# Optimization experiments

Hardware: AMD Instinct MI355X
Metric: run time of the kernel (lower is better)

## Reference

```python
import jax, jax.numpy as jnp
import numpy as np

NUM_BINS = 16
D_MODEL = 128
TAIL_BOUND = 20.0
MIN_BIN_WIDTH = 1e-3
MIN_BIN_HEIGHT = 1e-3
MIN_DERIVATIVE = 1e-3
EPS = 1e-6


def setup_inputs() -> dict:
    key = jax.random.key(0)
    ks = jax.random.split(key, 10)
    B, S = 32, 8192
    sc = 0.05  # small init scale so spline logits stay moderate
    return {
        "inputs": jax.random.normal(ks[0], (B, S), dtype=jnp.float32),
        "conditioning": jax.random.normal(ks[1], (B, S, D_MODEL), dtype=jnp.float32),
        "Ww": jax.random.normal(ks[2], (NUM_BINS, D_MODEL), dtype=jnp.float32) * sc,
        "bw": jax.random.normal(ks[3], (NUM_BINS,), dtype=jnp.float32) * sc,
        "Wh": jax.random.normal(ks[4], (NUM_BINS, D_MODEL), dtype=jnp.float32) * sc,
        "bh": jax.random.normal(ks[5], (NUM_BINS,), dtype=jnp.float32) * sc,
        "Wd": jax.random.normal(ks[6], (NUM_BINS - 1, D_MODEL), dtype=jnp.float32) * sc,
        "bd": jax.random.normal(ks[7], (NUM_BINS - 1,), dtype=jnp.float32) * sc,
        "Wl": jax.random.normal(ks[8], (NUM_BINS, D_MODEL), dtype=jnp.float32) * sc,
        "bl": jax.random.normal(ks[9], (NUM_BINS,), dtype=jnp.float32) * sc,
    }


def _rational_linear_spline(x, uw, uh, ud, ul, left, right, bottom, top):
    nb = uw.shape[-1]
    # bin widths / cumulative widths
    w = MIN_BIN_WIDTH + (1.0 - MIN_BIN_WIDTH * nb) * jax.nn.softmax(uw, axis=-1)
    cw = jnp.concatenate([jnp.zeros_like(w[..., :1]), jnp.cumsum(w, axis=-1)], axis=-1)
    cw = (right - left) * cw + left
    cw = cw.at[..., 0].set(left).at[..., -1].set(right)
    w = cw[..., 1:] - cw[..., :-1]
    # derivatives (ud already padded to nb+1 by caller)
    d = MIN_DERIVATIVE + jax.nn.softplus(ud)
    # bin heights / cumulative heights
    h = MIN_BIN_HEIGHT + (1.0 - MIN_BIN_HEIGHT * nb) * jax.nn.softmax(uh, axis=-1)
    ch = jnp.concatenate([jnp.zeros_like(h[..., :1]), jnp.cumsum(h, axis=-1)], axis=-1)
    ch = (top - bottom) * ch + bottom
    ch = ch.at[..., 0].set(bottom).at[..., -1].set(top)
    h = ch[..., 1:] - ch[..., :-1]
    # searchsorted via sum of comparisons (as in source)
    locs = cw.at[..., -1].add(EPS)
    idx = jnp.sum((x[..., None] >= locs).astype(jnp.int32), axis=-1) - 1
    idx = jnp.clip(idx, 0, nb - 1)
    g = lambda t: jnp.take_along_axis(t, idx[..., None], axis=-1)[..., 0]
    in_cw = g(cw)
    in_bw = g(w)
    in_ch = g(ch)
    in_delta = g(h / w)
    dk = g(d)
    dk1 = g(d[..., 1:])
    in_h = g(h)
    lambdas = 0.95 * jax.nn.sigmoid(ul) + 0.025
    lam = g(lambdas)
    wa = 1.0
    wb = jnp.sqrt(dk / dk1) * wa
    wc = (lam * wa * dk + (1.0 - lam) * wb * dk1) / in_delta
    ya = in_ch
    yb = in_h + in_ch
    yc = ((1.0 - lam) * wa * ya + lam * wb * yb) / ((1.0 - lam) * wa + lam * wb)
    theta = (x - in_cw) / in_bw
    m = theta <= lam
    num = jnp.where(m, wa * ya * (lam - theta) + wc * yc * theta,
                    wc * yc * (1.0 - theta) + wb * yb * (theta - lam))
    den = jnp.where(m, wa * (lam - theta) + wc * theta,
                    wc * (1.0 - theta) + wb * (theta - lam))
    out = num / den
    deriv_num = jnp.where(m, wa * wc * lam * (yc - ya), wb * wc * (1.0 - lam) * (yb - yc)) / in_bw
    logabsdet = jnp.log(deriv_num) - 2.0 * jnp.log(jnp.abs(den))
    return out, logabsdet


def reference(inputs, conditioning, Ww, bw, Wh, bh, Wd, bd, Wl, bl):
    # parameter nets (module.forward): note the module normalizes here AND the
    # spline normalizes again -- replicate faithfully.
    uw = jax.nn.softmax(jnp.einsum('bsd,kd->bsk', conditioning, Ww) + bw, axis=-1)
    uh = jax.nn.softmax(jnp.einsum('bsd,kd->bsk', conditioning, Wh) + bh, axis=-1)
    ud = jax.nn.softplus(jnp.einsum('bsd,kd->bsk', conditioning, Wd) + bd)
    ul = jax.nn.sigmoid(jnp.einsum('bsd,kd->bsk', conditioning, Wl) + bl)
    # linear tails: pad derivatives with constant so boundary derivative == 1
    const = float(np.log(np.exp(1.0 - MIN_DERIVATIVE) - 1.0))
    edge = jnp.full(ud.shape[:-1] + (1,), const, dtype=ud.dtype)
    udp = jnp.concatenate([edge, ud, edge], axis=-1)  # [B,S,nb+1]
    tb = TAIL_BOUND
    inside = (inputs >= -tb) & (inputs <= tb)
    xc = jnp.clip(inputs, -tb, tb)
    s_out, s_lad = _rational_linear_spline(xc, uw, uh, udp, ul, -tb, tb, -tb, tb)
    outputs = jnp.where(inside, s_out, inputs)
    logabsdet = jnp.where(inside, s_lad, 0.0)
    return outputs, logabsdet
```

## Files before the change

kernel.cpp:

```cpp
#include <hip/hip_runtime.h>
#include <math.h>

#define NB 16
#define DM 128
#define BM 256
#define ZSTRIDE 68

typedef _Float16 half8  __attribute__((ext_vector_type(8)));
typedef _Float16 half4v __attribute__((ext_vector_type(4)));
typedef _Float16 half2v __attribute__((ext_vector_type(2)));
typedef __fp16   fp16x2 __attribute__((ext_vector_type(2)));
typedef float    f32x4  __attribute__((ext_vector_type(4)));

__device__ __forceinline__ float frcp_(float x) { return __builtin_amdgcn_rcpf(x); }
__device__ __forceinline__ float softplus_fast(float x) {
    return fmaxf(x, 0.0f) + __logf(1.0f + __expf(-fabsf(x)));
}
__device__ __forceinline__ float sigmoid_fast(float x) {
    return frcp_(1.0f + __expf(-x));
}
__device__ __forceinline__ void softmax16_m(float* z) {
    float m = z[0];
#pragma unroll
    for (int k = 1; k < NB; k++) m = fmaxf(m, z[k]);
    float s = 0.0f;
#pragma unroll
    for (int k = 0; k < NB; k++) { z[k] = __expf(z[k] - m); s += z[k]; }
    float r = frcp_(s);
#pragma unroll
    for (int k = 0; k < NB; k++) z[k] *= r;
}
__device__ __forceinline__ void softmax16_nm(float* z) {
    float s = 0.0f;
#pragma unroll
    for (int k = 0; k < NB; k++) { z[k] = __expf(z[k]); s += z[k]; }
    float r = frcp_(s);
#pragma unroll
    for (int k = 0; k < NB; k++) z[k] *= r;
}

__device__ __forceinline__ half2v pk_(float lo, float hi) {
    fp16x2 p = __builtin_amdgcn_cvt_pkrtz(lo, hi);
    return __builtin_bit_cast(half2v, p);
}
__device__ __forceinline__ half8 cvt8(float4 a0, float4 a1) {
    half2v p0 = pk_(a0.x, a0.y);
    half2v p1 = pk_(a0.z, a0.w);
    half2v p2 = pk_(a1.x, a1.y);
    half2v p3 = pk_(a1.z, a1.w);
    half8 f;
    f[0] = p0[0]; f[1] = p0[1]; f[2] = p1[0]; f[3] = p1[1];
    f[4] = p2[0]; f[5] = p2[1]; f[6] = p3[0]; f[7] = p3[1];
    return f;
}

#define ISSUE(P, cr, koff)                                  \
    P##0 = *(const float4*)((cr) + (koff));                 \
    P##1 = *(const float4*)((cr) + (koff) + 4);             \
    P##2 = *(const float4*)((cr) + (koff) + 32);            \
    P##3 = *(const float4*)((cr) + (koff) + 36);

#define CVT2(P, lo, hi)                                     \
    lo = cvt8(P##0, P##1);                                  \
    hi = cvt8(P##2, P##3);

#define MFMA_S(af, s)                                                           \
    acc0 = __builtin_amdgcn_mfma_f32_16x16x32_f16(af, B0##s, acc0, 0, 0, 0);    \
    acc1 = __builtin_amdgcn_mfma_f32_16x16x32_f16(af, B1##s, acc1, 0, 0, 0);    \
    acc2 = __builtin_amdgcn_mfma_f32_16x16x32_f16(af, B2##s, acc2, 0, 0, 0);    \
    acc3 = __builtin_amdgcn_mfma_f32_16x16x32_f16(af, B3##s, acc3, 0, 0, 0);

#define STOREZ(c) {                                                             \
    _Float16* zpw = zbase + (size_t)((c) * 16) * ZSTRIDE;                       \
    _Pragma("unroll")                                                           \
    for (int r = 0; r < 4; r++) {                                               \
        half2v p0 = pk_(acc0[r], acc1[r]);                                      \
        half2v p1 = pk_(acc2[r], acc3[r]);                                      \
        half4v w; w[0] = p0[0]; w[1] = p0[1]; w[2] = p1[0]; w[3] = p1[1];       \
        *(half4v*)(zpw + (size_t)r * ZSTRIDE) = w;                              \
    } }

#define RESET_ACC  acc0 = zf4; acc1 = zf4; acc2 = zf4; acc3 = zf4;

#define STAGE_B(Wt, isWd, Q0, Q1, Q2, Q3) {                                     \
    const bool val = (!(isWd)) || (l15 < 15);                                   \
    const float* srcl = (Wt) + (size_t)(val ? l15 : 0) * DM + lg * 8;           \
    float4 q0 = *(const float4*)(srcl + 0),  q1 = *(const float4*)(srcl + 4);   \
    float4 q2 = *(const float4*)(srcl + 32), q3 = *(const float4*)(srcl + 36);  \
    float4 q4 = *(const float4*)(srcl + 64), q5 = *(const float4*)(srcl + 68);  \
    float4 q6 = *(const float4*)(srcl + 96), q7 = *(const float4*)(srcl + 100); \
    Q0 = val ? cvt8(q0, q1) : hz;                                               \
    Q1 = val ? cvt8(q2, q3) : hz;                                               \
    Q2 = val ? cvt8(q4, q5) : hz;                                               \
    Q3 = val ? cvt8(q6, q7) : hz; }

__global__ __launch_bounds__(256, 3) void spline_mfma(
    const float* __restrict__ xin, const float* __restrict__ cond,
    const float* __restrict__ Ww, const float* __restrict__ bw,
    const float* __restrict__ Wh, const float* __restrict__ bh,
    const float* __restrict__ Wd, const float* __restrict__ bd,
    const float* __restrict__ Wl, const float* __restrict__ bl,
    float* __restrict__ out, float* __restrict__ lad, int N)
{
    __shared__ __align__(16) _Float16 Z[BM * ZSTRIDE];

    const int tid  = threadIdx.x;
    const int wave = tid >> 6;
    const int lane = tid & 63;
    const int l15  = lane & 15;
    const int lg   = lane >> 4;
    const size_t blockRow = (size_t)blockIdx.x * BM;

    const size_t gi = blockRow + tid;
    float x = xin[gi < (size_t)N ? gi : 0];

    size_t gr0 = blockRow + (size_t)(wave * 64 + l15);
    size_t gr1 = gr0 + 16, gr2 = gr0 + 32, gr3 = gr0 + 48;
    if (gr0 >= (size_t)N) gr0 = (size_t)N - 1;
    if (gr1 >= (size_t)N) gr1 = (size_t)N - 1;
    if (gr2 >= (size_t)N) gr2 = (size_t)N - 1;
    if (gr3 >= (size_t)N) gr3 = (size_t)N - 1;
    const float* cr0 = cond + gr0 * DM + lg * 8;
    const float* cr1 = cond + gr1 * DM + lg * 8;
    const float* cr2 = cond + gr2 * DM + lg * 8;
    const float* cr3 = cond + gr3 * DM + lg * 8;

    float4 X0, X1, X2, X3, Y0, Y1, Y2, Y3;
    ISSUE(X, cr0, 0)
    ISSUE(Y, cr0, 64)

    half8 hz;
    hz[0]=hz[1]=hz[2]=hz[3]=hz[4]=hz[5]=hz[6]=hz[7] = (_Float16)0.0f;
    half8 B00, B01, B02, B03, B10, B11, B12, B13,
          B20, B21, B22, B23, B30, B31, B32, B33;
    STAGE_B(Ww, false, B00, B01, B02, B03)
    STAGE_B(Wh, false, B10, B11, B12, B13)
    STAGE_B(Wl, false, B20, B21, B22, B23)
    STAGE_B(Wd, true,  B30, B31, B32, B33)

    const f32x4 zf4 = {0.f, 0.f, 0.f, 0.f};
    f32x4 acc0 = zf4, acc1 = zf4, acc2 = zf4, acc3 = zf4;
    half8 af0, af1;
    _Float16* zbase = &Z[(size_t)(wave * 64 + lg * 4) * ZSTRIDE + l15 * 4];

    CVT2(X, af0, af1)
    ISSUE(X, cr1, 0)
    MFMA_S(af0, 0) MFMA_S(af1, 1)
    CVT2(Y, af0, af1)
    ISSUE(Y, cr1, 64)
    MFMA_S(af0, 2) MFMA_S(af1, 3)
    STOREZ(0) RESET_ACC

    CVT2(X, af0, af1)
    ISSUE(X, cr2, 0)
    MFMA_S(af0, 0) MFMA_S(af1, 1)
    CVT2(Y, af0, af1)
    ISSUE(Y, cr2, 64)
    MFMA_S(af0, 2) MFMA_S(af1, 3)
    STOREZ(1) RESET_ACC

    CVT2(X, af0, af1)
    ISSUE(X, cr3, 0)
    MFMA_S(af0, 0) MFMA_S(af1, 1)
    CVT2(Y, af0, af1)
    ISSUE(Y, cr3, 64)
    MFMA_S(af0, 2) MFMA_S(af1, 3)
    STOREZ(2) RESET_ACC

    CVT2(X, af0, af1)
    MFMA_S(af0, 0) MFMA_S(af1, 1)
    CVT2(Y, af0, af1)
    MFMA_S(af0, 2) MFMA_S(af1, 3)
    STOREZ(3)

    __builtin_amdgcn_sched_barrier(0);
    asm volatile("s_waitcnt lgkmcnt(0)" ::: "memory");
    __builtin_amdgcn_sched_barrier(0);

    if (gi >= (size_t)N) return;

    float zw[NB], zh[NB], zl[NB], zd[NB - 1];
    const half4v* zr4 = (const half4v*)&Z[(size_t)tid * ZSTRIDE];
#pragma unroll
    for (int j = 0; j < NB; j++) {
        half4v v = zr4[j];
        zw[j] = (float)v[0] + bw[j];
        zh[j] = (float)v[1] + bh[j];
        zl[j] = (float)v[2] + bl[j];
        if (j < NB - 1) zd[j] = (float)v[3] + bd[j];
    }

    float xc = fminf(fmaxf(x, -20.0f), 20.0f);

    softmax16_m(zw);
    softmax16_nm(zw);
    const float scale = (1.0f - 1e-3f * NB);
    float cw[NB + 1];
    cw[0] = -20.0f;
    float cum = 0.0f;
#pragma unroll
    for (int k = 0; k < NB; k++) {
        cum += 1e-3f + scale * zw[k];
        cw[k + 1] = 40.0f * cum - 20.0f;
    }
    cw[NB] = 20.0f;

    softmax16_m(zh);
    softmax16_nm(zh);
    float ch[NB + 1];
    ch[0] = -20.0f;
    cum = 0.0f;
#pragma unroll
    for (int k = 0; k < NB; k++) {
        cum += 1e-3f + scale * zh[k];
        ch[k + 1] = 40.0f * cum - 20.0f;
    }
    ch[NB] = 20.0f;

    float in_cw = cw[0], cw_hi = cw[1], in_ch = ch[0], ch_hi = ch[1];
    float zl_sel = zl[0], zd_lo = zd[0], zd_hi = zd[0];
#pragma unroll
    for (int k = 1; k < NB; k++) {
        bool take = (xc >= cw[k]);
        in_cw  = take ? cw[k]     : in_cw;
        cw_hi  = take ? cw[k + 1] : cw_hi;
        in_ch  = take ? ch[k]     : in_ch;
        ch_hi  = take ? ch[k + 1] : ch_hi;
        zl_sel = take ? zl[k]     : zl_sel;
        zd_lo  = take ? zd[k - 1] : zd_lo;
        zd_hi  = take ? zd[(k < NB - 1) ? k : NB - 2] : zd_hi;
    }
    bool firstbin = (xc <  cw[1]);
    bool lastbin  = (xc >= cw[NB - 1]);

    float in_bw = cw_hi - in_cw;
    float in_h  = ch_hi - in_ch;

    float dk  = firstbin ? 1.0f : (1e-3f + softplus_fast(softplus_fast(zd_lo)));
    float dk1 = lastbin  ? 1.0f : (1e-3f + softplus_fast(softplus_fast(zd_hi)));

    float ul  = sigmoid_fast(zl_sel);
    float lam = 0.95f * sigmoid_fast(ul) + 0.025f;

    float rbw = frcp_(in_bw);
    float in_delta = in_h * rbw;
    float wb = sqrtf(dk * frcp_(dk1));
    float wc = (lam * dk + (1.0f - lam) * wb * dk1) * frcp_(in_delta);
    float ya = in_ch;
    float yb = in_h + in_ch;
    float yc = ((1.0f - lam) * ya + lam * wb * yb) * frcp_((1.0f - lam) + lam * wb);
    float theta = (xc - in_cw) * rbw;
    bool mlt = (theta <= lam);

    float num = mlt ? (ya * (lam - theta) + wc * yc * theta)
                    : (wc * yc * (1.0f - theta) + wb * yb * (theta - lam));
    float den = mlt ? ((lam - theta) + wc * theta)
                    : (wc * (1.0f - theta) + wb * (theta - lam));
    float sout = num * frcp_(den);
    float dnum = (mlt ? (wc * lam * (yc - ya))
                      : (wb * wc * (1.0f - lam) * (yb - yc))) * rbw;
    float slad = __logf(dnum) - 2.0f * __logf(fabsf(den));

    bool inside = (x >= -20.0f) && (x <= 20.0f);
    out[gi] = inside ? sout : x;
    lad[gi] = inside ? slad : 0.0f;
}

extern "C" void kernel_launch(void* const* d_in, const int* in_sizes, int n_in,
                              void* d_out, int out_size, void* d_ws, size_t ws_size,
                              hipStream_t stream) {
    const float* xin  = (const float*)d_in[0];
    const float* cond = (const float*)d_in[1];
    const float* Ww   = (const float*)d_in[2];
    const float* bwp  = (const float*)d_in[3];
    const float* Wh   = (const float*)d_in[4];
    const float* bhp  = (const float*)d_in[5];
    const float* Wd   = (const float*)d_in[6];
    const float* bdp  = (const float*)d_in[7];
    const float* Wl   = (const float*)d_in[8];
    const float* blp  = (const float*)d_in[9];
    int N = in_sizes[0];
    float* out = (float*)d_out;
    float* lad = out + N;
    int grid = (N + BM - 1) / BM;
    hipLaunchKernelGGL(spline_mfma, dim3(grid), dim3(256), 0, stream,
                       xin, cond, Ww, bwp, Wh, bhp, Wd, bdp, Wl, blp, out, lad, N);
}
```

Baseline: 41.63 us.

## Issue all conditioning loads up front and relax launch bounds to two blocks

Measured after the change: 39.08 us. 1.07x faster.

```diff
diff --git a/kernel.cpp b/kernel.cpp
--- a/kernel.cpp
+++ b/kernel.cpp
@@ -54,15 +54,21 @@
     return f;
 }
 
-#define ISSUE(P, cr, koff)                                  \
-    P##0 = *(const float4*)((cr) + (koff));                 \
-    P##1 = *(const float4*)((cr) + (koff) + 4);             \
-    P##2 = *(const float4*)((cr) + (koff) + 32);            \
-    P##3 = *(const float4*)((cr) + (koff) + 36);
-
-#define CVT2(P, lo, hi)                                     \
-    lo = cvt8(P##0, P##1);                                  \
-    hi = cvt8(P##2, P##3);
+#define LOADC(c)                                        \
+    A##c##_0 = *(const float4*)(cr##c + 0);             \
+    A##c##_1 = *(const float4*)(cr##c + 4);             \
+    A##c##_2 = *(const float4*)(cr##c + 32);            \
+    A##c##_3 = *(const float4*)(cr##c + 36);            \
+    A##c##_4 = *(const float4*)(cr##c + 64);            \
+    A##c##_5 = *(const float4*)(cr##c + 68);            \
+    A##c##_6 = *(const float4*)(cr##c + 96);            \
+    A##c##_7 = *(const float4*)(cr##c + 100);
+
+#define CVTC(c)                                         \
+    af0 = cvt8(A##c##_0, A##c##_1);                     \
+    af1 = cvt8(A##c##_2, A##c##_3);                     \
+    af2 = cvt8(A##c##_4, A##c##_5);                     \
+    af3 = cvt8(A##c##_6, A##c##_7);
 
 #define MFMA_S(af, s)                                                           \
     acc0 = __builtin_amdgcn_mfma_f32_16x16x32_f16(af, B0##s, acc0, 0, 0, 0);    \
@@ -94,7 +100,7 @@
     Q2 = val ? cvt8(q4, q5) : hz;                                               \
     Q3 = val ? cvt8(q6, q7) : hz; }
 
-__global__ __launch_bounds__(256, 3) void spline_mfma(
+__global__ __launch_bounds__(256, 2) void spline_mfma(
     const float* __restrict__ xin, const float* __restrict__ cond,
     const float* __restrict__ Ww, const float* __restrict__ bw,
     const float* __restrict__ Wh, const float* __restrict__ bh,
@@ -110,9 +116,16 @@
     const int l15  = lane & 15;
     const int lg   = lane >> 4;
     const size_t blockRow = (size_t)blockIdx.x * BM;
-
     const size_t gi = blockRow + tid;
-    float x = xin[gi < (size_t)N ? gi : 0];
+
+    half8 hz;
+    hz[0]=hz[1]=hz[2]=hz[3]=hz[4]=hz[5]=hz[6]=hz[7] = (_Float16)0.0f;
+    half8 B00, B01, B02, B03, B10, B11, B12, B13,
+          B20, B21, B22, B23, B30, B31, B32, B33;
+    STAGE_B(Ww, false, B00, B01, B02, B03)
+    STAGE_B(Wh, false, B10, B11, B12, B13)
+    STAGE_B(Wl, false, B20, B21, B22, B23)
+    STAGE_B(Wd, true,  B30, B31, B32, B33)
 
     size_t gr0 = blockRow + (size_t)(wave * 64 + l15);
     size_t gr1 = gr0 + 16, gr2 = gr0 + 32, gr3 = gr0 + 48;
@@ -125,52 +138,32 @@
     const float* cr2 = cond + gr2 * DM + lg * 8;
     const float* cr3 = cond + gr3 * DM + lg * 8;
 
-    float4 X0, X1, X2, X3, Y0, Y1, Y2, Y3;
-    ISSUE(X, cr0, 0)
-    ISSUE(Y, cr0, 64)
-
-    half8 hz;
-    hz[0]=hz[1]=hz[2]=hz[3]=hz[4]=hz[5]=hz[6]=hz[7] = (_Float16)0.0f;
-    half8 B00, B01, B02, B03, B10, B11, B12, B13,
-          B20, B21, B22, B23, B30, B31, B32, B33;
-    STAGE_B(Ww, false, B00, B01, B02, B03)
-    STAGE_B(Wh, false, B10, B11, B12, B13)
-    STAGE_B(Wl, false, B20, B21, B22, B23)
-    STAGE_B(Wd, true,  B30, B31, B32, B33)
+    float4 A0_0, A0_1, A0_2, A0_3, A0_4, A0_5, A0_6, A0_7;
+    float4 A1_0, A1_1, A1_2, A1_3, A1_4, A1_5, A1_6, A1_7;
+    float4 A2_0, A2_1, A2_2, A2_3, A2_4, A2_5, A2_6, A2_7;
+    float4 A3_0, A3_1, A3_2, A3_3, A3_4, A3_5, A3_6, A3_7;
+    LOADC(0)
+    LOADC(1)
+    LOADC(2)
+    LOADC(3)
+    float x = xin[gi < (size_t)N ? gi : 0];
 
     const f32x4 zf4 = {0.f, 0.f, 0.f, 0.f};
     f32x4 acc0 = zf4, acc1 = zf4, acc2 = zf4, acc3 = zf4;
-    half8 af0, af1;
+    half8 af0, af1, af2, af3;
     _Float16* zbase = &Z[(size_t)(wave * 64 + lg * 4) * ZSTRIDE + l15 * 4];
 
-    CVT2(X, af0, af1)
-    ISSUE(X, cr1, 0)
-    MFMA_S(af0, 0) MFMA_S(af1, 1)
-    CVT2(Y, af0, af1)
-    ISSUE(Y, cr1, 64)
-    MFMA_S(af0, 2) MFMA_S(af1, 3)
+    CVTC(0)
+    MFMA_S(af0, 0) MFMA_S(af1, 1) MFMA_S(af2, 2) MFMA_S(af3, 3)
     STOREZ(0) RESET_ACC
-
-    CVT2(X, af0, af1)
-    ISSUE(X, cr2, 0)
-    MFMA_S(af0, 0) MFMA_S(af1, 1)
-    CVT2(Y, af0, af1)
-    ISSUE(Y, cr2, 64)
-    MFMA_S(af0, 2) MFMA_S(af1, 3)
+    CVTC(1)
+    MFMA_S(af0, 0) MFMA_S(af1, 1) MFMA_S(af2, 2) MFMA_S(af3, 3)
     STOREZ(1) RESET_ACC
-
-    CVT2(X, af0, af1)
-    ISSUE(X, cr3, 0)
-    MFMA_S(af0, 0) MFMA_S(af1, 1)
-    CVT2(Y, af0, af1)
-    ISSUE(Y, cr3, 64)
-    MFMA_S(af0, 2) MFMA_S(af1, 3)
+    CVTC(2)
+    MFMA_S(af0, 0) MFMA_S(af1, 1) MFMA_S(af2, 2) MFMA_S(af3, 3)
     STOREZ(2) RESET_ACC
-
-    CVT2(X, af0, af1)
-    MFMA_S(af0, 0) MFMA_S(af1, 1)
-    CVT2(Y, af0, af1)
-    MFMA_S(af0, 2) MFMA_S(af1, 3)
+    CVTC(3)
+    MFMA_S(af0, 0) MFMA_S(af1, 1) MFMA_S(af2, 2) MFMA_S(af3, 3)
     STOREZ(3)
 
     __builtin_amdgcn_sched_barrier(0);
```
